# Performance work log

Hardware: AMD Instinct MI355X
Metric: run time of the kernel (lower is better)

Reference implementation:

```python
import jax, jax.numpy as jnp
import numpy as np

DN = ('NCHW', 'OIHW', 'NCHW')

def conv2d(x, w, b):
    y = jax.lax.conv_general_dilated(x, w, window_strides=(1, 1), padding='VALID', dimension_numbers=DN)
    return y + b[None, :, None, None]

def setup_inputs() -> dict:
    key = jax.random.key(0)
    ks = jax.random.split(key, 16)
    s = 0.02  # small init scale to keep relu chains numerically tame
    B, Cin, OUT = 128, 4, 9
    return {
        'state_m': jax.random.normal(ks[0], (B, Cin, 100, 100), jnp.float32),
        'state_g': jax.random.normal(ks[1], (B, 2), jnp.float32),
        'state_v': jax.random.normal(ks[2], (B, 2), jnp.float32),
        'conv1_w': jax.random.normal(ks[3], (32, Cin, 32, 32), jnp.float32) * s,
        'conv1_b': jnp.zeros((32,), jnp.float32),
        'conv2_w': jax.random.normal(ks[4], (64, 32, 32, 32), jnp.float32) * s,
        'conv2_b': jnp.zeros((64,), jnp.float32),
        'conv3_w': jax.random.normal(ks[5], (64, 64, 8, 8), jnp.float32) * s,
        'conv3_b': jnp.zeros((64,), jnp.float32),
        'conv4_w': jax.random.normal(ks[6], (64, 64, 8, 8), jnp.float32) * s,
        'conv4_b': jnp.zeros((64,), jnp.float32),
        'fc1_w': jax.random.normal(ks[7], (67, 4), jnp.float32) * s,
        'fc1_b': jnp.zeros((67,), jnp.float32),
        'fc2_w': jax.random.normal(ks[8], (512, 6400), jnp.float32) * s,
        'fc2_b': jnp.zeros((512,), jnp.float32),
        'fc3_w': jax.random.normal(ks[9], (512, 512), jnp.float32) * s,
        'fc3_b': jnp.zeros((512,), jnp.float32),
        'fc4_ea_w': jax.random.normal(ks[10], (OUT, 512), jnp.float32) * s,
        'fc4_ea_b': jnp.zeros((OUT,), jnp.float32),
        'fc4_ev_w': jax.random.normal(ks[11], (1, 512), jnp.float32) * s,
        'fc4_ev_b': jnp.zeros((1,), jnp.float32),
    }

def reference(state_m, state_g, state_v,
              conv1_w, conv1_b, conv2_w, conv2_b, conv3_w, conv3_b, conv4_w, conv4_b,
              fc1_w, fc1_b, fc2_w, fc2_b, fc3_w, fc3_b,
              fc4_ea_w, fc4_ea_b, fc4_ev_w, fc4_ev_b):
    x_m = jax.nn.relu(conv2d(state_m, conv1_w, conv1_b))   # [B,32,69,69]
    x_m = jax.nn.relu(conv2d(x_m, conv2_w, conv2_b))       # [B,64,38,38]
    x_m = jax.nn.relu(conv2d(x_m, conv3_w, conv3_b))       # [B,64,31,31]
    x_gv_ = jax.nn.relu(jnp.concatenate([state_g, state_v], axis=1) @ fc1_w.T + fc1_b)  # [B,67]
    convw = x_m.shape[2]  # 31
    # Torch loop overwrites x_gv each iteration: final tile is filled with x_gv_[0, convw-1]
    scalar = x_gv_[0, convw - 1]
    x_pls = x_m + scalar  # broadcast add (the CPU round-trip tile in torch)
    x_pls = jax.nn.relu(conv2d(x_pls, conv4_w, conv4_b))   # [B,64,24,24]
    x_pls = jax.nn.relu(conv2d(x_pls, conv4_w, conv4_b))   # [B,64,17,17]
    x_pls = jax.nn.relu(conv2d(x_pls, conv4_w, conv4_b))   # [B,64,10,10]
    x = x_pls.reshape(x_pls.shape[0], -1)                  # [B,6400]
    x = jax.nn.relu(x @ fc2_w.T + fc2_b)
    x = jax.nn.relu(x @ fc3_w.T + fc3_b)
    adv = x @ fc4_ea_w.T + fc4_ea_b                        # [B,outputs]
    val = x @ fc4_ev_w.T + fc4_ev_b                        # [B,1]
    return adv + val - jnp.mean(adv, axis=1, keepdims=True)
```

## Files before the change

### kernel.cpp

```cpp
#include <hip/hip_runtime.h>
#include <stdint.h>


using bf16_t = __bf16;
using bf16x8 = __attribute__((ext_vector_type(8))) __bf16;
using bf16x4 = __attribute__((ext_vector_type(4))) __bf16;
using f32x4  = __attribute__((ext_vector_type(4))) float;
using f32x16 = __attribute__((ext_vector_type(16))) float;

__device__ __forceinline__ f32x4 mfma16(bf16x8 a, bf16x8 b, f32x4 c) {
    return __builtin_amdgcn_mfma_f32_16x16x32_bf16(a, b, c, 0, 0, 0);
}
__device__ __forceinline__ f32x16 mfma32(bf16x8 a, bf16x8 b, f32x16 c) {
    return __builtin_amdgcn_mfma_f32_32x32x16_bf16(a, b, c, 0, 0, 0);
}

template<bool A16>
__device__ __forceinline__ bf16x8 load_frag(const bf16_t* p) {
    if constexpr (A16) {
        return *reinterpret_cast<const bf16x8*>(p);
    } else {
        union { bf16x8 v; uint64_t u[2]; } r;
        r.u[0] = *reinterpret_cast<const uint64_t*>(p);
        r.u[1] = *reinterpret_cast<const uint64_t*>(p + 4);
        return r.v;
    }
}

template<int CIN>
__global__ void pack_w(const float* __restrict__ src, bf16_t* __restrict__ dst,
                       int COUT, int KK) {
    int total = COUT * KK;
    for (int t = blockIdx.x * blockDim.x + threadIdx.x; t < total;
         t += gridDim.x * blockDim.x) {
        int cout = t / KK;
        int khw  = t - cout * KK;
        alignas(16) bf16_t tmp[CIN];
        #pragma unroll
        for (int c = 0; c < CIN; ++c)
            tmp[c] = (bf16_t)src[((size_t)cout * CIN + c) * KK + khw];
        bf16_t* d = dst + (size_t)t * CIN;
        if constexpr (CIN == 1) {
            d[0] = tmp[0];
        } else if constexpr (CIN == 4) {
            *reinterpret_cast<uint2*>(d) = *reinterpret_cast<const uint2*>(tmp);
        } else {
            #pragma unroll
            for (int c = 0; c < CIN; c += 8)
                *reinterpret_cast<uint4*>(d + c) =
                    *reinterpret_cast<const uint4*>(tmp + c);
        }
    }
}

template<int CIN, int COUT, int K>
__global__ void pack_wA(const float* __restrict__ src, bf16_t* __restrict__ dst) {
    constexpr int S  = K * CIN / 16;
    constexpr int NT = COUT / 32;
    int t = blockIdx.x * 256 + threadIdx.x;
    int l  = t & 63;
    int f  = t >> 6;
    int n  = f % NT;
    int fs = f / NT;
    int s  = fs % S;
    int kh = fs / S;
    if (kh >= K) return;
    int cout = n * 32 + (l & 31);
    int k0   = s * 16 + (l >> 5) * 8;
    alignas(16) bf16_t tmp[8];
    #pragma unroll
    for (int e = 0; e < 8; ++e) {
        int k   = k0 + e;
        int kw  = k / CIN;
        int cin = k % CIN;
        tmp[e] = (bf16_t)src[(((size_t)cout * CIN + cin) * K + kh) * K + kw];
    }
    *reinterpret_cast<uint4*>(dst + (size_t)t * 8) =
        *reinterpret_cast<const uint4*>(tmp);
}

__global__ void fc1_scalar(const float* __restrict__ g, const float* __restrict__ v,
                           const float* __restrict__ w, const float* __restrict__ b,
                           float* __restrict__ outp) {
    if (threadIdx.x == 0 && blockIdx.x == 0) {
        float s = b[30] + g[0] * w[120] + g[1] * w[121] + v[0] * w[122] + v[1] * w[123];
        *outp = s > 0.f ? s : 0.f;
    }
}

template<int CIN, int COUT, int W, int K, int OW, int WMT, int NSLOT,
         int ADD_SCALAR, int DEPTH>
__global__ __launch_bounds__(256, 2) void conv_rr(
    const bf16_t* __restrict__ in, const bf16_t* __restrict__ wA,
    const float* __restrict__ bias, bf16_t* __restrict__ out,
    const float* __restrict__ scal) {
    constexpr int  P     = OW * OW;
    constexpr int  PIXB  = CIN * 2;
    constexpr int  ROWB  = W * PIXB;
    constexpr bool TR    = (CIN >= 16);
    constexpr int  NCH   = TR ? PIXB / 16 : 1;
    constexpr int  SPP   = TR ? NCH / 2 : 1;
    constexpr int  PS    = TR ? (W + 1) * 16 : 0;
    constexpr int  SLOTB0 = TR ? NCH * PS : ROWB;
    constexpr int  PADB  = TR ? ((16 * OW - SLOTB0) % 128 + 128) % 128 : 0;
    constexpr int  SLOTB = SLOTB0 + PADB;
    constexpr int  LDSB  = NSLOT * SLOTB;
    constexpr int  S     = K * CIN / 16;
    constexpr int  NT    = COUT / 32;
    constexpr int  BPX   = WMT * 32 * 4;
    constexpr int  CH    = ROWB / 16;
    constexpr int  NLD   = (CH + 255) / 256;
    __shared__ __align__(16) char smem[LDSB];

    const int tid  = threadIdx.x;
    const int wave = tid >> 6, lane = tid & 63;
    const int l31  = lane & 31, h = lane >> 5;
    const int img  = blockIdx.z;
    const int p0   = blockIdx.x * BPX;

    const char* inb = (const char*)(in + (size_t)img * ((size_t)W * W * CIN));

    const int r0 = p0 / OW;
    int plast = p0 + BPX - 1; if (plast > P - 1) plast = P - 1;
    const int r1 = plast / OW;

    int woff[NLD];
    #pragma unroll
    for (int i = 0; i < NLD; ++i) {
        int c = i * 256 + tid;
        if (c < CH) woff[i] = TR ? (c % NCH) * PS + (c / NCH) * 16 : c * 16;
        else        woff[i] = 0;
    }

    int pix[WMT], ldsadr[WMT];
    #pragma unroll
    for (int m = 0; m < WMT; ++m) {
        int p  = p0 + (wave * WMT + m) * 32 + l31;
        pix[m] = p;
        int pc = p < P ? p : P - 1;
        int oh = pc / OW;
        int ow = pc - oh * OW;
        ldsadr[m] = (oh % NSLOT) * SLOTB +
                    (TR ? ow * 16 + h * PS : ow * PIXB + h * 16);
    }

    for (int r = r0; r <= r1; ++r) {
        const char* g = inb + (size_t)r * ROWB;
        int base = (r % NSLOT) * SLOTB;
        for (int c = tid; c < CH; c += 256) {
            bf16x8 v = *reinterpret_cast<const bf16x8*>(g + c * 16);
            int off = TR ? (c % NCH) * PS + (c / NCH) * 16 : c * 16;
            *reinterpret_cast<bf16x8*>(smem + base + off) = v;
        }
    }
    __syncthreads();

    f32x16 acc[WMT][NT] = {};

    int wsl = (r1 + 1) % NSLOT;
    const char* gpre = inb + (size_t)(r1 + 1) * ROWB;
    const bf16_t* wl = wA + lane * 8;

    for (int kh = 0; kh < K; ++kh) {
        bf16x8 stv[NLD];
        const bool pf = kh < K - 1;
        const bf16_t* ap = wl + (size_t)kh * (S * NT * 512);

#define STVISSUE                                                            \
        if (pf) {                                                           \
            _Pragma("unroll")                                               \
            for (int i = 0; i < NLD; ++i) {                                 \
                int c = i * 256 + tid;                                      \
                if (c < CH) stv[i] = *reinterpret_cast<const bf16x8*>(gpre + c * 16); \
            }                                                               \
        }

        if constexpr (DEPTH == 4) {
            bf16x8 bS0[WMT], bS1[WMT], bS2[WMT], bS3[WMT];
            bf16x8 aS0[NT],  aS1[NT],  aS2[NT],  aS3[NT];

#define LOADSET(BS, AS, SIDX)                                               \
            {                                                               \
                const int _s = (SIDX);                                      \
                _Pragma("unroll")                                           \
                for (int m = 0; m < WMT; ++m) {                             \
                    int a = TR ? ldsadr[m] + (_s % SPP) * (2 * PS) + (_s / SPP) * 16 \
                               : ldsadr[m] + _s * 32;                       \
                    BS[m] = *reinterpret_cast<const bf16x8*>(smem + a);     \
                }                                                           \
                _Pragma("unroll")                                           \
                for (int n = 0; n < NT; ++n)                                \
                    AS[n] = *reinterpret_cast<const bf16x8*>(ap + (_s * NT + n) * 512); \
            }
#define MFMASET(BS, AS)                                                     \
            {                                                               \
                __builtin_amdgcn_s_setprio(1);                              \
                _Pragma("unroll")                                           \
                for (int m = 0; m < WMT; ++m)                               \
                    _Pragma("unroll")                                       \
                    for (int n = 0; n < NT; ++n)                            \
                        acc[m][n] = mfma32(AS[n], BS[m], acc[m][n]);        \
                __builtin_amdgcn_s_setprio(0);                              \
            }

            LOADSET(bS0, aS0, 0)
            LOADSET(bS1, aS1, 1)
            LOADSET(bS2, aS2, 2)
            MFMASET(bS0, aS0)  LOADSET(bS3, aS3, 3)
            MFMASET(bS1, aS1)  LOADSET(bS0, aS0, 4)
            MFMASET(bS2, aS2)  LOADSET(bS1, aS1, 5)
            MFMASET(bS3, aS3)  LOADSET(bS2, aS2, 6)
            STVISSUE
            for (int sb = 4; sb + 8 <= S; sb += 4) {
                MFMASET(bS0, aS0)  LOADSET(bS3, aS3, sb + 3)
                MFMASET(bS1, aS1)  LOADSET(bS0, aS0, sb + 4)
                MFMASET(bS2, aS2)  LOADSET(bS1, aS1, sb + 5)
                MFMASET(bS3, aS3)  LOADSET(bS2, aS2, sb + 6)
            }
            MFMASET(bS0, aS0)  LOADSET(bS3, aS3, S - 1)
            MFMASET(bS1, aS1)
            MFMASET(bS2, aS2)
            MFMASET(bS3, aS3)
#undef LOADSET
#undef MFMASET
        } else {
            auto bread = [&](int m, int s) -> bf16x8 {
                int a = TR ? ldsadr[m] + (s % SPP) * (2 * PS) + (s / SPP) * 16
                           : ldsadr[m] + s * 32;
                return *reinterpret_cast<const bf16x8*>(smem + a);
            };
            bf16x8 bcur[WMT], acur[NT];
            #pragma unroll
            for (int m = 0; m < WMT; ++m) bcur[m] = bread(m, 0);
            #pragma unroll
            for (int n = 0; n < NT; ++n)
                acur[n] = *reinterpret_cast<const bf16x8*>(ap + n * 512);

            #pragma unroll
            for (int s = 0; s < S - 1; ++s) {
                bf16x8 bnx[WMT], anx[NT];
                #pragma unroll
                for (int m = 0; m < WMT; ++m) bnx[m] = bread(m, s + 1);
                #pragma unroll
                for (int n = 0; n < NT; ++n)
                    anx[n] = *reinterpret_cast<const bf16x8*>(ap + ((s + 1) * NT + n) * 512);
                if (s == 2) { STVISSUE }
                #pragma unroll
                for (int m = 0; m < WMT; ++m)
                    #pragma unroll
                    for (int n = 0; n < NT; ++n)
                        acc[m][n] = mfma32(acur[n], bcur[m], acc[m][n]);
                #pragma unroll
                for (int m = 0; m < WMT; ++m) bcur[m] = bnx[m];
                #pragma unroll
                for (int n = 0; n < NT; ++n) acur[n] = anx[n];
            }
            #pragma unroll
            for (int m = 0; m < WMT; ++m)
                #pragma unroll
                for (int n = 0; n < NT; ++n)
                    acc[m][n] = mfma32(acur[n], bcur[m], acc[m][n]);
        }
#undef STVISSUE

        if (pf) {
            int wb0 = wsl * SLOTB;
            #pragma unroll
            for (int i = 0; i < NLD; ++i) {
                int c = i * 256 + tid;
                if (c < CH)
                    *reinterpret_cast<bf16x8*>(smem + wb0 + woff[i]) = stv[i];
            }
            gpre += ROWB;
            wsl = (wsl + 1 == NSLOT) ? 0 : wsl + 1;
        }
        __syncthreads();
        #pragma unroll
        for (int m = 0; m < WMT; ++m) {
            int a2 = ldsadr[m] + SLOTB;
            ldsadr[m] = a2 >= LDSB ? a2 - LDSB : a2;
        }
    }

    float sc = 0.f;
    if constexpr (ADD_SCALAR) sc = *scal;
    bf16_t* outb = out + (size_t)img * ((size_t)P * COUT);
    #pragma unroll
    for (int m = 0; m < WMT; ++m) {
        if (pix[m] < P) {
            #pragma unroll
            for (int n = 0; n < NT; ++n) {
                #pragma unroll
                for (int rg = 0; rg < 4; ++rg) {
                    int cb = n * 32 + rg * 8 + h * 4;
                    f32x4 bv = *reinterpret_cast<const f32x4*>(bias + cb);
                    union { bf16x4 v; uint2 u; } o;
                    #pragma unroll
                    for (int j = 0; j < 4; ++j) {
                        float x = acc[m][n][rg * 4 + j] + bv[j];
                        x = x > 0.f ? x : 0.f;
                        x += sc;
                        o.v[j] = (bf16_t)x;
                    }
                    *reinterpret_cast<uint2*>(outb + (size_t)pix[m] * COUT + cb) = o.u;
                }
            }
        }
    }
}

template<int CIN, int COUT, int W, int K, int OW, int NBLK, int WMT,
         int ADD_SCALAR, bool A16>
__global__ __launch_bounds__(256, 2) void conv_mfma(
    const bf16_t* __restrict__ in, const bf16_t* __restrict__ wp,
    const float* __restrict__ bias, bf16_t* __restrict__ out,
    const float* __restrict__ scal) {
    constexpr int P    = OW * OW;
    constexpr int KCIN = K * CIN;
    constexpr int KTOT = K * KCIN;
    constexpr int RS   = KCIN / 32;
    constexpr int NT   = NBLK / 16;
    constexpr int BMT  = WMT * 4;

    const int b     = blockIdx.z;
    const int cout0 = blockIdx.y * NBLK;
    const int wave  = threadIdx.x >> 6;
    const int lane  = threadIdx.x & 63;
    const int l15   = lane & 15;
    const int l4    = lane >> 4;
    const int mt0   = blockIdx.x * BMT + wave * WMT;

    const bf16_t* inb = in + (size_t)b * (W * W * CIN);

    int      pix[WMT];
    uint32_t pb[WMT];
    #pragma unroll
    for (int m = 0; m < WMT; ++m) {
        int p  = (mt0 + m) * 16 + l15;
        pix[m] = p;
        int pc = p < P ? p : P - 1;
        int oh = pc / OW;
        int ow = pc - oh * OW;
        pb[m]  = (uint32_t)(oh * W + ow) * CIN;
    }
    uint32_t wb[NT];
    #pragma unroll
    for (int n = 0; n < NT; ++n)
        wb[n] = (uint32_t)(cout0 + n * 16 + l15) * KTOT + (uint32_t)l4 * 8u;

    f32x4 acc[WMT][NT];
    #pragma unroll
    for (int m = 0; m < WMT; ++m)
        #pragma unroll
        for (int n = 0; n < NT; ++n)
            acc[m][n] = f32x4{0.f, 0.f, 0.f, 0.f};

    uint32_t bofs = (uint32_t)l4 * 8u;
    for (int kh = 0; kh < K; ++kh) {
        #pragma unroll
        for (int s = 0; s < RS; ++s) {
            bf16x8 af[NT];
            #pragma unroll
            for (int n = 0; n < NT; ++n)
                af[n] = load_frag<true>(wp + wb[n] + kh * KCIN + s * 32);
            #pragma unroll
            for (int m = 0; m < WMT; ++m) {
                bf16x8 bfr = load_frag<A16>(inb + pb[m] + bofs + s * 32);
                #pragma unroll
                for (int n = 0; n < NT; ++n)
                    acc[m][n] = mfma16(af[n], bfr, acc[m][n]);
            }
        }
        bofs += (uint32_t)(W * CIN);
    }

    float sc = 0.f;
    if constexpr (ADD_SCALAR) sc = *scal;
    bf16_t* outb = out + (size_t)b * P * COUT;
    #pragma unroll
    for (int n = 0; n < NT; ++n) {
        const int cb = cout0 + n * 16 + l4 * 4;
        f32x4 bv = *reinterpret_cast<const f32x4*>(bias + cb);
        #pragma unroll
        for (int m = 0; m < WMT; ++m) {
            if (pix[m] < P) {
                f32x4 v = acc[m][n];
                union { bf16x4 h; uint2 u; } st;
                #pragma unroll
                for (int r = 0; r < 4; ++r) {
                    float x = v[r] + bv[r];
                    x = x > 0.f ? x : 0.f;
                    x += sc;
                    st.h[r] = (bf16_t)x;
                }
                *reinterpret_cast<uint2*>(outb + (size_t)pix[m] * COUT + cb) = st.u;
            }
        }
    }
}

__global__ __launch_bounds__(256, 2) void fc2_kernel(
    const bf16_t* __restrict__ x, const bf16_t* __restrict__ w,
    float* __restrict__ part) {
    const int nb = blockIdx.x, kc = blockIdx.y;
    const int wave = threadIdx.x >> 6, lane = threadIdx.x & 63;
    const int l15 = lane & 15, l4 = lane >> 4;
    const int wm = wave & 1, wn = wave >> 1;

    f32x4 acc[4][2];
    #pragma unroll
    for (int m = 0; m < 4; ++m)
        #pragma unroll
        for (int n = 0; n < 2; ++n) acc[m][n] = f32x4{0.f, 0.f, 0.f, 0.f};

    uint32_t xb[4], wbf[2];
    #pragma unroll
    for (int m = 0; m < 4; ++m)
        xb[m] = (uint32_t)(16 * (wm * 4 + m) + l15) * 6400u + kc * 1600u + l4 * 8u;
    #pragma unroll
    for (int n = 0; n < 2; ++n)
        wbf[n] = (uint32_t)(nb * 64 + wn * 32 + n * 16 + l15) * 6400u + kc * 1600u + l4 * 8u;

    for (int s = 0; s < 50; ++s) {
        bf16x8 af[2];
        #pragma unroll
        for (int n = 0; n < 2; ++n)
            af[n] = load_frag<true>(w + wbf[n] + s * 32);
        #pragma unroll
        for (int m = 0; m < 4; ++m) {
            bf16x8 bfr = load_frag<true>(x + xb[m] + s * 32);
            #pragma unroll
            for (int n = 0; n < 2; ++n)
                acc[m][n] = mfma16(af[n], bfr, acc[m][n]);
        }
    }
    #pragma unroll
    for (int m = 0; m < 4; ++m) {
        int bcol = 16 * (wm * 4 + m) + l15;
        #pragma unroll
        for (int n = 0; n < 2; ++n) {
            int cf = nb * 64 + wn * 32 + n * 16 + l4 * 4;
            *reinterpret_cast<f32x4*>(part + ((size_t)kc * 128 + bcol) * 512 + cf) =
                acc[m][n];
        }
    }
}

__global__ void fc2_reduce(const float* __restrict__ part,
                           const float* __restrict__ bias,
                           bf16_t* __restrict__ xo) {
    int t = blockIdx.x * 256 + threadIdx.x;
    if (t < 128 * 512) {
        int b = t >> 9, co = t & 511;
        float s = bias[co];
        #pragma unroll
        for (int kc = 0; kc < 4; ++kc) s += part[((size_t)kc * 128 + b) * 512 + co];
        xo[t] = (bf16_t)(s > 0.f ? s : 0.f);
    }
}

__global__ __launch_bounds__(256, 2) void fc3_kernel(
    const bf16_t* __restrict__ x, const bf16_t* __restrict__ w,
    const float* __restrict__ bias, bf16_t* __restrict__ xo) {
    const int nb = blockIdx.x;
    const int wave = threadIdx.x >> 6, lane = threadIdx.x & 63;
    const int l15 = lane & 15, l4 = lane >> 4;

    f32x4 acc[2][4];
    #pragma unroll
    for (int m = 0; m < 2; ++m)
        #pragma unroll
        for (int n = 0; n < 4; ++n) acc[m][n] = f32x4{0.f, 0.f, 0.f, 0.f};

    uint32_t xb[2], wbf[4];
    #pragma unroll
    for (int m = 0; m < 2; ++m)
        xb[m] = (uint32_t)(16 * (wave * 2 + m) + l15) * 512u + l4 * 8u;
    #pragma unroll
    for (int n = 0; n < 4; ++n)
        wbf[n] = (uint32_t)(nb * 64 + n * 16 + l15) * 512u + l4 * 8u;

    #pragma unroll
    for (int s = 0; s < 16; ++s) {
        bf16x8 af[4];
        #pragma unroll
        for (int n = 0; n < 4; ++n) af[n] = load_frag<true>(w + wbf[n] + s * 32);
        #pragma unroll
        for (int m = 0; m < 2; ++m) {
            bf16x8 bfr = load_frag<true>(x + xb[m] + s * 32);
            #pragma unroll
            for (int n = 0; n < 4; ++n)
                acc[m][n] = mfma16(af[n], bfr, acc[m][n]);
        }
    }
    #pragma unroll
    for (int n = 0; n < 4; ++n) {
        int cf = nb * 64 + n * 16 + l4 * 4;
        f32x4 bv = *reinterpret_cast<const f32x4*>(bias + cf);
        #pragma unroll
        for (int m = 0; m < 2; ++m) {
            int brow = 16 * (wave * 2 + m) + l15;
            union { bf16x4 h; uint2 u; } st;
            #pragma unroll
            for (int r = 0; r < 4; ++r) {
                float v = acc[m][n][r] + bv[r];
                st.h[r] = (bf16_t)(v > 0.f ? v : 0.f);
            }
            *reinterpret_cast<uint2*>(xo + (size_t)brow * 512 + cf) = st.u;
        }
    }
}

__global__ void final_kernel(const bf16_t* __restrict__ x,
                             const float* __restrict__ eaw, const float* __restrict__ eab,
                             const float* __restrict__ evw, const float* __restrict__ evb,
                             float* __restrict__ out) {
    int b = blockIdx.x, lane = threadIdx.x;
    bf16x8 xv = *reinterpret_cast<const bf16x8*>(x + (size_t)b * 512 + lane * 8);
    float xs[8];
    #pragma unroll
    for (int i = 0; i < 8; ++i) xs[i] = (float)xv[i];
    float a[10];
    #pragma unroll
    for (int j = 0; j < 10; ++j) {
        const float* wr = (j < 9) ? (eaw + (size_t)j * 512) : evw;
        const f32x4* w4 = reinterpret_cast<const f32x4*>(wr + lane * 8);
        f32x4 w0 = w4[0], w1 = w4[1];
        float s = 0.f;
        #pragma unroll
        for (int i = 0; i < 4; ++i) s += xs[i] * w0[i];
        #pragma unroll
        for (int i = 0; i < 4; ++i) s += xs[4 + i] * w1[i];
        a[j] = s;
    }
    #pragma unroll
    for (int off = 1; off < 64; off <<= 1)
        #pragma unroll
        for (int j = 0; j < 10; ++j) a[j] += __shfl_xor(a[j], off);
    if (lane < 9) {
        float val  = a[9] + evb[0];
        float mean = 0.f;
        #pragma unroll
        for (int j = 0; j < 9; ++j) mean += a[j] + eab[j];
        mean *= (1.f / 9.f);
        out[b * 9 + lane] = a[lane] + eab[lane] + val - mean;
    }
}

extern "C" void kernel_launch(void* const* d_in, const int* in_sizes, int n_in,
                              void* d_out, int out_size, void* d_ws, size_t ws_size,
                              hipStream_t stream) {
    const float* state_m  = (const float*)d_in[0];
    const float* state_g  = (const float*)d_in[1];
    const float* state_v  = (const float*)d_in[2];
    const float* conv1_w  = (const float*)d_in[3];
    const float* conv1_b  = (const float*)d_in[4];
    const float* conv2_w  = (const float*)d_in[5];
    const float* conv2_b  = (const float*)d_in[6];
    const float* conv3_w  = (const float*)d_in[7];
    const float* conv3_b  = (const float*)d_in[8];
    const float* conv4_w  = (const float*)d_in[9];
    const float* conv4_b  = (const float*)d_in[10];
    const float* fc1_w    = (const float*)d_in[11];
    const float* fc1_b    = (const float*)d_in[12];
    const float* fc2_w    = (const float*)d_in[13];
    const float* fc2_b    = (const float*)d_in[14];
    const float* fc3_w    = (const float*)d_in[15];
    const float* fc3_b    = (const float*)d_in[16];
    const float* fc4_ea_w = (const float*)d_in[17];
    const float* fc4_ea_b = (const float*)d_in[18];
    const float* fc4_ev_w = (const float*)d_in[19];
    const float* fc4_ev_b = (const float*)d_in[20];

    char* ws = (char*)d_ws;
    bf16_t* w1A    = (bf16_t*)(ws + 0);
    bf16_t* w2A    = (bf16_t*)(ws + 262144);
    bf16_t* w3A    = (bf16_t*)(ws + 4456448);
    bf16_t* w4A    = (bf16_t*)(ws + 4980736);
    bf16_t* w4p    = (bf16_t*)(ws + 5505024);
    bf16_t* fc2wp  = (bf16_t*)(ws + 6029312);
    bf16_t* fc3wp  = (bf16_t*)(ws + 12582912);
    float*  scal   = (float*) (ws + 13107200);
    float*  part   = (float*) (ws + 13107456);
    bf16_t* x2fc   = (bf16_t*)(ws + 14156032);
    bf16_t* x3fc   = (bf16_t*)(ws + 14287104);
    bf16_t* a0     = (bf16_t*)(ws + 14418176);
    bf16_t* x4a    = (bf16_t*)(ws + 14418176);
    bf16_t* x1     = (bf16_t*)(ws + 24658176);
    bf16_t* x4b    = (bf16_t*)(ws + 24658176);
    bf16_t* x4c    = (bf16_t*)(ws + 29393152);
    bf16_t* x2     = (bf16_t*)(ws + 63660288);
    bf16_t* x3     = (bf16_t*)(ws + 87318784);
    (void)in_sizes; (void)n_in; (void)out_size; (void)ws_size;

    pack_wA<4, 32, 32> <<<dim3(64),   256, 0, stream>>>(conv1_w, w1A);
    pack_wA<32, 64, 32><<<dim3(1024), 256, 0, stream>>>(conv2_w, w2A);
    pack_wA<64, 64, 8> <<<dim3(128),  256, 0, stream>>>(conv3_w, w3A);
    pack_wA<64, 64, 8> <<<dim3(128),  256, 0, stream>>>(conv4_w, w4A);
    pack_w<64><<<dim3(16),   256, 0, stream>>>(conv4_w, w4p, 64, 64);
    pack_w<64><<<dim3(200),  256, 0, stream>>>(fc2_w, fc2wp, 512, 100);
    pack_w<1> <<<dim3(1024), 256, 0, stream>>>(fc3_w, fc3wp, 512, 512);
    pack_w<4> <<<dim3(1024), 256, 0, stream>>>(state_m, a0, 128, 10000);
    fc1_scalar<<<1, 64, 0, stream>>>(state_g, state_v, fc1_w, fc1_b, scal);

    conv_rr<4, 32, 100, 32, 69, 3, 8, 0, 1>
        <<<dim3(13, 1, 128), 256, 0, stream>>>(a0, w1A, conv1_b, x1, nullptr);
    conv_rr<32, 64, 69, 32, 38, 2, 9, 0, 4>
        <<<dim3(6, 1, 128), 256, 0, stream>>>(x1, w2A, conv2_b, x2, nullptr);
    conv_rr<64, 64, 38, 8, 31, 2, 11, 1, 1>
        <<<dim3(4, 1, 128), 256, 0, stream>>>(x2, w3A, conv3_b, x3, scal);
    conv_rr<64, 64, 31, 8, 24, 2, 13, 0, 1>
        <<<dim3(3, 1, 128), 256, 0, stream>>>(x3, w4A, conv4_b, x4a, nullptr);
    conv_rr<64, 64, 24, 8, 17, 2, 17, 0, 1>
        <<<dim3(2, 1, 128), 256, 0, stream>>>(x4a, w4A, conv4_b, x4b, nullptr);
    conv_mfma<64, 64, 17, 8, 10, 32, 1, 0, true>
        <<<dim3(2, 2, 128), 256, 0, stream>>>(x4b, w4p, conv4_b, x4c, nullptr);

    fc2_kernel<<<dim3(8, 4), 256, 0, stream>>>(x4c, fc2wp, part);
    fc2_reduce<<<dim3(256), 256, 0, stream>>>(part, fc2_b, x2fc);
    fc3_kernel<<<dim3(8), 256, 0, stream>>>(x2fc, fc3wp, fc3_b, x3fc);
    final_kernel<<<dim3(128), 64, 0, stream>>>(x3fc, fc4_ea_w, fc4_ea_b,
                                               fc4_ev_w, fc4_ev_b, (float*)d_out);
}
```

Measured before the change: 1.177 ms.

## Add dedicated conv2 kernel with larger pixel tiles and four-row LDS staging

Replaces the generic conv_rr instance for conv2 with a specialized kernel that uses three 32-pixel tiles per wave (384 pixels per block, 4 blocks per image instead of 6) and a 16-slot LDS ring. It prefetches and stores four input rows per sync step instead of one, so there are fewer block barriers per output tile. The goal is to reuse each weight fragment across more pixels and to amortize synchronization. In exchange it uses more LDS (about 73KB) and more registers, which may limit occupancy, and the generic kernel's DEPTH-4 pipeline path is removed.

```diff
diff --git a/kernel.cpp b/kernel.cpp
--- a/kernel.cpp
+++ b/kernel.cpp
@@ -88,8 +88,175 @@
     }
 }
 
+__global__ __launch_bounds__(256, 2) void conv2_k4(
+    const bf16_t* __restrict__ in, const bf16_t* __restrict__ wA,
+    const float* __restrict__ bias, bf16_t* __restrict__ out) {
+    constexpr int W = 69, OW = 38, CIN = 32;
+    constexpr int P    = OW * OW;
+    constexpr int ROWB = W * CIN * 2;
+    constexpr int PS   = (W + 1) * 16;
+    constexpr int SLOTB = 4576;
+    constexpr int NSLOT = 16;
+    constexpr int LDSB  = NSLOT * SLOTB;
+    constexpr int S = 64, NT = 2, WMT = 3;
+    constexpr int BPX = 384;
+    constexpr int CHR = ROWB / 16;
+    constexpr int CH4 = 4 * CHR;
+    __shared__ __align__(16) char smem[LDSB];
+
+    const int tid  = threadIdx.x;
+    const int wave = tid >> 6, lane = tid & 63;
+    const int l31  = lane & 31, h = lane >> 5;
+    const int img  = blockIdx.z;
+    const int p0   = blockIdx.x * BPX;
+
+    const char* inb = (const char*)(in + (size_t)img * (W * W * CIN));
+    const int r0 = p0 / OW;
+    int plast = p0 + BPX - 1; if (plast > P - 1) plast = P - 1;
+    const int r1 = plast / OW;
+
+    int pix[WMT], ldsadr[WMT];
+    #pragma unroll
+    for (int m = 0; m < WMT; ++m) {
+        int p  = p0 + (wave * WMT + m) * 32 + l31;
+        pix[m] = p;
+        int pc = p < P ? p : P - 1;
+        int oh = pc / OW;
+        int ow = pc - oh * OW;
+        ldsadr[m] = (oh & 15) * SLOTB + ow * 16 + h * PS;
+    }
+
+    for (int r = r0; r <= r1 + 3; ++r) {
+        const char* g = inb + (size_t)r * ROWB;
+        int base = (r & 15) * SLOTB;
+        for (int c = tid; c < CHR; c += 256)
+            *reinterpret_cast<bf16x8*>(smem + base + (c & 3) * PS + (c >> 2) * 16) =
+                *reinterpret_cast<const bf16x8*>(g + c * 16);
+    }
+    __syncthreads();
+
+    f32x16 acc[WMT][NT] = {};
+    int wsl = (r1 + 4) & 15;
+    const char* gpre = inb + (size_t)(r1 + 4) * ROWB;
+    const bf16_t* wl = wA + lane * 8;
+
+    for (int kp = 0; kp < 8; ++kp) {
+        const bool pf = kp < 7;
+        bf16x8 stv[5];
+
+#define STVISSUE                                                            \
+        if (pf) {                                                           \
+            _Pragma("unroll")                                               \
+            for (int i = 0; i < 5; ++i) {                                   \
+                int c = i * 256 + tid;                                      \
+                if (c < CH4) stv[i] = *reinterpret_cast<const bf16x8*>(gpre + c * 16); \
+            }                                                               \
+        }
+
+        #pragma unroll
+        for (int kl = 0; kl < 4; ++kl) {
+            const bf16_t* ap = wl + (size_t)(kp * 4 + kl) * (S * NT * 512);
+            int adr[WMT];
+            #pragma unroll
+            for (int m = 0; m < WMT; ++m) {
+                int a = ldsadr[m] + kl * SLOTB;
+                adr[m] = a >= LDSB ? a - LDSB : a;
+            }
+
+            bf16x8 bS0[WMT], bS1[WMT], bS2[WMT], bS3[WMT];
+            bf16x8 aS0[NT],  aS1[NT],  aS2[NT],  aS3[NT];
+
+#define LOADSET(BS, AS, SIDX)                                               \
+            {                                                               \
+                const int _s = (SIDX);                                      \
+                _Pragma("unroll")                                           \
+                for (int m = 0; m < WMT; ++m)                               \
+                    BS[m] = *reinterpret_cast<const bf16x8*>(                \
+                        smem + adr[m] + (_s & 1) * (2 * PS) + (_s >> 1) * 16); \
+                _Pragma("unroll")                                           \
+                for (int n = 0; n < NT; ++n)                                \
+                    AS[n] = *reinterpret_cast<const bf16x8*>(ap + (_s * NT + n) * 512); \
+            }
+#define MFMASET(BS, AS)                                                     \
+            {                                                               \
+                __builtin_amdgcn_s_setprio(1);                              \
+                _Pragma("unroll")                                           \
+                for (int m = 0; m < WMT; ++m)                               \
+                    _Pragma("unroll")                                       \
+                    for (int n = 0; n < NT; ++n)                            \
+                        acc[m][n] = mfma32(AS[n], BS[m], acc[m][n]);        \
+                __builtin_amdgcn_s_setprio(0);                              \
+            }
+
+            LOADSET(bS0, aS0, 0)
+            LOADSET(bS1, aS1, 1)
+            LOADSET(bS2, aS2, 2)
+            MFMASET(bS0, aS0)  LOADSET(bS3, aS3, 3)
+            MFMASET(bS1, aS1)  LOADSET(bS0, aS0, 4)
+            MFMASET(bS2, aS2)  LOADSET(bS1, aS1, 5)
+            MFMASET(bS3, aS3)  LOADSET(bS2, aS2, 6)
+            if (kl == 0) { STVISSUE }
+            for (int sb = 4; sb + 8 <= S; sb += 4) {
+                MFMASET(bS0, aS0)  LOADSET(bS3, aS3, sb + 3)
+                MFMASET(bS1, aS1)  LOADSET(bS0, aS0, sb + 4)
+                MFMASET(bS2, aS2)  LOADSET(bS1, aS1, sb + 5)
+                MFMASET(bS3, aS3)  LOADSET(bS2, aS2, sb + 6)
+            }
+            MFMASET(bS0, aS0)  LOADSET(bS3, aS3, S - 1)
+            MFMASET(bS1, aS1)
+            MFMASET(bS2, aS2)
+            MFMASET(bS3, aS3)
+#undef LOADSET
+#undef MFMASET
+        }
+#undef STVISSUE
+
+        if (pf) {
+            #pragma unroll
+            for (int i = 0; i < 5; ++i) {
+                int c = i * 256 + tid;
+                if (c < CH4) {
+                    int j = c / CHR, u = c - j * CHR;
+                    *reinterpret_cast<bf16x8*>(
+                        smem + ((wsl + j) & 15) * SLOTB + (u & 3) * PS + (u >> 2) * 16) = stv[i];
+                }
+            }
+            gpre += 4 * ROWB;
+            wsl = (wsl + 4) & 15;
+        }
+        __syncthreads();
+        #pragma unroll
+        for (int m = 0; m < WMT; ++m) {
+            int a2 = ldsadr[m] + 4 * SLOTB;
+            ldsadr[m] = a2 >= LDSB ? a2 - LDSB : a2;
+        }
+    }
+
+    bf16_t* outb = out + (size_t)img * ((size_t)P * 64);
+    #pragma unroll
+    for (int m = 0; m < WMT; ++m) {
+        if (pix[m] < P) {
+            #pragma unroll
+            for (int n = 0; n < NT; ++n) {
+                #pragma unroll
+                for (int rg = 0; rg < 4; ++rg) {
+                    int cb = n * 32 + rg * 8 + h * 4;
+                    f32x4 bv = *reinterpret_cast<const f32x4*>(bias + cb);
+                    union { bf16x4 v; uint2 u; } o;
+                    #pragma unroll
+                    for (int j = 0; j < 4; ++j) {
+                        float x = acc[m][n][rg * 4 + j] + bv[j];
+                        o.v[j] = (bf16_t)(x > 0.f ? x : 0.f);
+                    }
+                    *reinterpret_cast<uint2*>(outb + (size_t)pix[m] * 64 + cb) = o.u;
+                }
+            }
+        }
+    }
+}
+
 template<int CIN, int COUT, int W, int K, int OW, int WMT, int NSLOT,
-         int ADD_SCALAR, int DEPTH>
+         int ADD_SCALAR>
 __global__ __launch_bounds__(256, 2) void conv_rr(
     const bf16_t* __restrict__ in, const bf16_t* __restrict__ wA,
     const float* __restrict__ bias, bf16_t* __restrict__ out,
@@ -166,102 +333,48 @@
         const bool pf = kh < K - 1;
         const bf16_t* ap = wl + (size_t)kh * (S * NT * 512);
 
-#define STVISSUE                                                            \
-        if (pf) {                                                           \
-            _Pragma("unroll")                                               \
-            for (int i = 0; i < NLD; ++i) {                                 \
-                int c = i * 256 + tid;                                      \
-                if (c < CH) stv[i] = *reinterpret_cast<const bf16x8*>(gpre + c * 16); \
-            }                                                               \
-        }
-
-        if constexpr (DEPTH == 4) {
-            bf16x8 bS0[WMT], bS1[WMT], bS2[WMT], bS3[WMT];
-            bf16x8 aS0[NT],  aS1[NT],  aS2[NT],  aS3[NT];
-
-#define LOADSET(BS, AS, SIDX)                                               \
-            {                                                               \
-                const int _s = (SIDX);                                      \
-                _Pragma("unroll")                                           \
-                for (int m = 0; m < WMT; ++m) {                             \
-                    int a = TR ? ldsadr[m] + (_s % SPP) * (2 * PS) + (_s / SPP) * 16 \
-                               : ldsadr[m] + _s * 32;                       \
-                    BS[m] = *reinterpret_cast<const bf16x8*>(smem + a);     \
-                }                                                           \
-                _Pragma("unroll")                                           \
-                for (int n = 0; n < NT; ++n)                                \
-                    AS[n] = *reinterpret_cast<const bf16x8*>(ap + (_s * NT + n) * 512); \
-            }
-#define MFMASET(BS, AS)                                                     \
-            {                                                               \
-                __builtin_amdgcn_s_setprio(1);                              \
-                _Pragma("unroll")                                           \
-                for (int m = 0; m < WMT; ++m)                               \
-                    _Pragma("unroll")                                       \
-                    for (int n = 0; n < NT; ++n)                            \
-                        acc[m][n] = mfma32(AS[n], BS[m], acc[m][n]);        \
-                __builtin_amdgcn_s_setprio(0);                              \
-            }
-
-            LOADSET(bS0, aS0, 0)
-            LOADSET(bS1, aS1, 1)
-            LOADSET(bS2, aS2, 2)
-            MFMASET(bS0, aS0)  LOADSET(bS3, aS3, 3)
-            MFMASET(bS1, aS1)  LOADSET(bS0, aS0, 4)
-            MFMASET(bS2, aS2)  LOADSET(bS1, aS1, 5)
-            MFMASET(bS3, aS3)  LOADSET(bS2, aS2, 6)
-            STVISSUE
-            for (int sb = 4; sb + 8 <= S; sb += 4) {
-                MFMASET(bS0, aS0)  LOADSET(bS3, aS3, sb + 3)
-                MFMASET(bS1, aS1)  LOADSET(bS0, aS0, sb + 4)
-                MFMASET(bS2, aS2)  LOADSET(bS1, aS1, sb + 5)
-                MFMASET(bS3, aS3)  LOADSET(bS2, aS2, sb + 6)
-            }
-            MFMASET(bS0, aS0)  LOADSET(bS3, aS3, S - 1)
-            MFMASET(bS1, aS1)
-            MFMASET(bS2, aS2)
-            MFMASET(bS3, aS3)
-#undef LOADSET
-#undef MFMASET
-        } else {
-            auto bread = [&](int m, int s) -> bf16x8 {
-                int a = TR ? ldsadr[m] + (s % SPP) * (2 * PS) + (s / SPP) * 16
-                           : ldsadr[m] + s * 32;
-                return *reinterpret_cast<const bf16x8*>(smem + a);
-            };
-            bf16x8 bcur[WMT], acur[NT];
-            #pragma unroll
-            for (int m = 0; m < WMT; ++m) bcur[m] = bread(m, 0);
+        auto bread = [&](int m, int s) -> bf16x8 {
+            int a = TR ? ldsadr[m] + (s % SPP) * (2 * PS) + (s / SPP) * 16
+                       : ldsadr[m] + s * 32;
+            return *reinterpret_cast<const bf16x8*>(smem + a);
+        };
+        bf16x8 bcur[WMT], acur[NT];
+        #pragma unroll
+        for (int m = 0; m < WMT; ++m) bcur[m] = bread(m, 0);
+        #pragma unroll
+        for (int n = 0; n < NT; ++n)
+            acur[n] = *reinterpret_cast<const bf16x8*>(ap + n * 512);
+
+        #pragma unroll
+        for (int s = 0; s < S - 1; ++s) {
+            bf16x8 bnx[WMT], anx[NT];
+            #pragma unroll
+            for (int m = 0; m < WMT; ++m) bnx[m] = bread(m, s + 1);
             #pragma unroll
             for (int n = 0; n < NT; ++n)
-                acur[n] = *reinterpret_cast<const bf16x8*>(ap + n * 512);
-
-            #pragma unroll
-            for (int s = 0; s < S - 1; ++s) {
-                bf16x8 bnx[WMT], anx[NT];
+                anx[n] = *reinterpret_cast<const bf16x8*>(ap + ((s + 1) * NT + n) * 512);
+            if (s == 2 && pf) {
                 #pragma unroll
-                for (int m = 0; m < WMT; ++m) bnx[m] = bread(m, s + 1);
-                #pragma unroll
-                for (int n = 0; n < NT; ++n)
-                    anx[n] = *reinterpret_cast<const bf16x8*>(ap + ((s + 1) * NT + n) * 512);
-                if (s == 2) { STVISSUE }
-                #pragma unroll
-                for (int m = 0; m < WMT; ++m)
-                    #pragma unroll
-                    for (int n = 0; n < NT; ++n)
-                        acc[m][n] = mfma32(acur[n], bcur[m], acc[m][n]);
-                #pragma unroll
-                for (int m = 0; m < WMT; ++m) bcur[m] = bnx[m];
-                #pragma unroll
-                for (int n = 0; n < NT; ++n) acur[n] = anx[n];
+                for (int i = 0; i < NLD; ++i) {
+                    int c = i * 256 + tid;
+                    if (c < CH) stv[i] = *reinterpret_cast<const bf16x8*>(gpre + c * 16);
+                }
             }
             #pragma unroll
             for (int m = 0; m < WMT; ++m)
                 #pragma unroll
                 for (int n = 0; n < NT; ++n)
                     acc[m][n] = mfma32(acur[n], bcur[m], acc[m][n]);
-        }
-#undef STVISSUE
+            #pragma unroll
+            for (int m = 0; m < WMT; ++m) bcur[m] = bnx[m];
+            #pragma unroll
+            for (int n = 0; n < NT; ++n) acur[n] = anx[n];
+        }
+        #pragma unroll
+        for (int m = 0; m < WMT; ++m)
+            #pragma unroll
+            for (int n = 0; n < NT; ++n)
+                acc[m][n] = mfma32(acur[n], bcur[m], acc[m][n]);
 
         if (pf) {
             int wb0 = wsl * SLOTB;
@@ -603,15 +716,14 @@
     pack_w<4> <<<dim3(1024), 256, 0, stream>>>(state_m, a0, 128, 10000);
     fc1_scalar<<<1, 64, 0, stream>>>(state_g, state_v, fc1_w, fc1_b, scal);
 
-    conv_rr<4, 32, 100, 32, 69, 3, 8, 0, 1>
+    conv_rr<4, 32, 100, 32, 69, 3, 8, 0>
         <<<dim3(13, 1, 128), 256, 0, stream>>>(a0, w1A, conv1_b, x1, nullptr);
-    conv_rr<32, 64, 69, 32, 38, 2, 9, 0, 4>
-        <<<dim3(6, 1, 128), 256, 0, stream>>>(x1, w2A, conv2_b, x2, nullptr);
-    conv_rr<64, 64, 38, 8, 31, 2, 11, 1, 1>
+    conv2_k4<<<dim3(4, 1, 128), 256, 0, stream>>>(x1, w2A, conv2_b, x2);
+    conv_rr<64, 64, 38, 8, 31, 2, 11, 1>
         <<<dim3(4, 1, 128), 256, 0, stream>>>(x2, w3A, conv3_b, x3, scal);
-    conv_rr<64, 64, 31, 8, 24, 2, 13, 0, 1>
+    conv_rr<64, 64, 31, 8, 24, 2, 13, 0>
         <<<dim3(3, 1, 128), 256, 0, stream>>>(x3, w4A, conv4_b, x4a, nullptr);
-    conv_rr<64, 64, 24, 8, 17, 2, 17, 0, 1>
+    conv_rr<64, 64, 24, 8, 17, 2, 17, 0>
         <<<dim3(2, 1, 128), 256, 0, stream>>>(x4a, w4A, conv4_b, x4b, nullptr);
     conv_mfma<64, 64, 17, 8, 10, 32, 1, 0, true>
         <<<dim3(2, 2, 128), 256, 0, stream>>>(x4b, w4p, conv4_b, x4c, nullptr);
```

New measurement: 1.146 ms. 1.03x faster.
